# Optimization experiments

Hardware: AMD Instinct MI355X
Metric: run time of the kernel (lower is better)

The kernel has to match this reference:

```python
import jax, jax.numpy as jnp
import numpy as np

# RReLU in eval mode is leaky_relu with slope = (lower+upper)/2 = (1/8 + 1/3)/2
RRELU_SLOPE = (1.0 / 8.0 + 1.0 / 3.0) / 2.0  # = 11/48

N_NODES, FEAT_DIM = 100000, 512
EMBED_DIM = 256
BATCH, NUM_SAMPLE = 16384, 10


def setup_inputs() -> dict:
    key = jax.random.key(0)
    k1, k2, k3 = jax.random.split(key, 3)
    features = jax.random.normal(k1, (N_NODES, FEAT_DIM), dtype=jnp.float32)
    # Xavier-uniform-style init for the weight [embed_dim, feat_dim]
    bound = float(np.sqrt(6.0 / (EMBED_DIM + FEAT_DIM)))
    weight = jax.random.uniform(k2, (EMBED_DIM, FEAT_DIM), dtype=jnp.float32,
                                minval=-bound, maxval=bound)
    # Pre-sampled neighbor ids per batch node: [BATCH, NUM_SAMPLE]
    neigh_idx = jax.random.randint(k3, (BATCH, NUM_SAMPLE), 0, N_NODES, dtype=jnp.int64)
    return {"features": features, "weight": weight, "neigh_idx": neigh_idx}


def reference(features, weight, neigh_idx):
    # Mean aggregator: gather sampled neighbor features and average -> [B, F]
    agg = jnp.take(features, neigh_idx, axis=0).mean(axis=1)
    # weight.mm(agg.t()) -> [E, B]
    y = jnp.einsum("ef,bf->eb", weight, agg)
    # RReLU (eval mode): leaky with mean slope
    return jnp.where(y >= 0, y, y * RRELU_SLOPE)
```

## Files before the change

kernel.cpp:

```cpp
#include <hip/hip_runtime.h>
#include <stdint.h>

constexpr int FEAT  = 512;
constexpr int EMB   = 256;
constexpr int BATCH = 16384;
constexpr int NSAMP = 10;
constexpr int NB    = 32;
constexpr float SLOPE  = 11.0f / 48.0f;
constexpr float INV_NS = 1.0f / 10.0f;

using f32x4 = __attribute__((ext_vector_type(4))) float;
using frag8 = __attribute__((ext_vector_type(8))) short;

static __device__ __forceinline__ unsigned f2b(float x) {
    unsigned u = __builtin_bit_cast(unsigned, x);
    return (u + 0x7fffu + ((u >> 16) & 1u)) >> 16;
}
static __device__ __forceinline__ unsigned pk2(float lo, float hi) {
    return f2b(lo) | (f2b(hi) << 16);
}

__global__ __launch_bounds__(256, 2) void enc_fused(const float* __restrict__ feat,
                                                    const float* __restrict__ wgt,
                                                    const int*   __restrict__ idx,
                                                    float*       __restrict__ out) {
    __shared__ ushort Bs[NB * FEAT];

    const int tid = threadIdx.x;
    const int n0  = blockIdx.x * NB;

    {
        const int r   = tid >> 3;
        const int sub = tid & 7;
        const int* ib = idx + (size_t)(n0 + r) * NSAMP;
        const float* base[NSAMP];
#pragma unroll
        for (int j = 0; j < NSAMP; ++j)
            base[j] = feat + (size_t)ib[j] * FEAT;
        const int swz = (r & 7) << 4;
#pragma unroll
        for (int c = 0; c < 16; ++c) {
            const int col4 = c * 8 + sub;
            float sx = 0.f, sy = 0.f, sz = 0.f, sw = 0.f;
#pragma unroll
            for (int j = 0; j < NSAMP; ++j) {
                const float4 v = *reinterpret_cast<const float4*>(base[j] + col4 * 4);
                sx += v.x; sy += v.y; sz += v.z; sw += v.w;
            }
            ushort4 o;
            o.x = (ushort)f2b(sx * INV_NS); o.y = (ushort)f2b(sy * INV_NS);
            o.z = (ushort)f2b(sz * INV_NS); o.w = (ushort)f2b(sw * INV_NS);
            const int kb = (col4 * 8) ^ swz;
            *reinterpret_cast<ushort4*>((char*)Bs + r * (FEAT * 2) + kb) = o;
        }
    }
    __syncthreads();

    const int wv   = tid >> 6;
    const int lane = tid & 63;
    const int l15  = lane & 15, lq = lane >> 4;
    const int mb   = wv * 64;

    f32x4 acc[4][2] = {};

#pragma unroll
    for (int k0 = 0; k0 < FEAT; k0 += 32) {
        frag8 af[4], bf[2];
#pragma unroll
        for (int i = 0; i < 4; ++i) {
            const float* wp = wgt + (size_t)(mb + i * 16 + l15) * FEAT + k0 + lq * 8;
            const float4 a0 = *reinterpret_cast<const float4*>(wp);
            const float4 a1 = *reinterpret_cast<const float4*>(wp + 4);
            union { frag8 f; unsigned u[4]; } pk;
            pk.u[0] = pk2(a0.x, a0.y);
            pk.u[1] = pk2(a0.z, a0.w);
            pk.u[2] = pk2(a1.x, a1.y);
            pk.u[3] = pk2(a1.z, a1.w);
            af[i] = pk.f;
        }
#pragma unroll
        for (int j = 0; j < 2; ++j) {
            const int row = j * 16 + l15;
            const int kb  = (k0 * 2 + lq * 16) ^ ((row & 7) << 4);
            bf[j] = *reinterpret_cast<const frag8*>((const char*)Bs + row * (FEAT * 2) + kb);
        }
#pragma unroll
        for (int i = 0; i < 4; ++i)
#pragma unroll
            for (int j = 0; j < 2; ++j)
                acc[i][j] = __builtin_amdgcn_mfma_f32_16x16x32_bf16(af[i], bf[j], acc[i][j], 0, 0, 0);
    }

#pragma unroll
    for (int i = 0; i < 4; ++i) {
        const int rb = mb + i * 16 + lq * 4;
#pragma unroll
        for (int j = 0; j < 2; ++j) {
            const int col = n0 + j * 16 + l15;
#pragma unroll
            for (int q = 0; q < 4; ++q) {
                float y = acc[i][j][q];
                y = (y >= 0.f) ? y : y * SLOPE;
                out[(size_t)(rb + q) * BATCH + col] = y;
            }
        }
    }
}

extern "C" void kernel_launch(void* const* d_in, const int* in_sizes, int n_in,
                              void* d_out, int out_size, void* d_ws, size_t ws_size,
                              hipStream_t stream) {
    const float* feat = (const float*)d_in[0];
    const float* wgt  = (const float*)d_in[1];
    const int*   idx  = (const int*)d_in[2];
    float*       out  = (float*)d_out;

    enc_fused<<<BATCH / NB, 256, 0, stream>>>(feat, wgt, idx, out);
}
```

Measured before the change: 75.90 us.

## Double batch tile to 64 nodes with 512 threads and wave-per-row gather

Each block now handles 64 batch nodes with 8 waves instead of 32 nodes with 4 waves. The gather changes so that one wave reads a whole neighbor row as contiguous 32-byte chunks per lane and writes packed bf16 straight to shared memory. The MFMA tiling becomes 32x64 per wave instead of 64x32, so the weight matrix is re-read and re-converted half as often across the grid. The cost is double the LDS per block (64KB), which may limit how many blocks fit on each CU, and half as many blocks in the grid.

```diff
diff --git a/kernel.cpp b/kernel.cpp
--- a/kernel.cpp
+++ b/kernel.cpp
@@ -5,7 +5,7 @@
 constexpr int EMB   = 256;
 constexpr int BATCH = 16384;
 constexpr int NSAMP = 10;
-constexpr int NB    = 32;
+constexpr int NB    = 64;
 constexpr float SLOPE  = 11.0f / 48.0f;
 constexpr float INV_NS = 1.0f / 10.0f;
 
@@ -20,82 +20,78 @@
     return f2b(lo) | (f2b(hi) << 16);
 }
 
-__global__ __launch_bounds__(256, 2) void enc_fused(const float* __restrict__ feat,
+__global__ __launch_bounds__(512, 2) void enc_fused(const float* __restrict__ feat,
                                                     const float* __restrict__ wgt,
                                                     const int*   __restrict__ idx,
                                                     float*       __restrict__ out) {
     __shared__ ushort Bs[NB * FEAT];
 
-    const int tid = threadIdx.x;
-    const int n0  = blockIdx.x * NB;
+    const int tid  = threadIdx.x;
+    const int wv   = tid >> 6;
+    const int lane = tid & 63;
+    const int n0   = blockIdx.x * NB;
 
-    {
-        const int r   = tid >> 3;
-        const int sub = tid & 7;
-        const int* ib = idx + (size_t)(n0 + r) * NSAMP;
-        const float* base[NSAMP];
+#pragma unroll 2
+    for (int rr = 0; rr < 8; ++rr) {
+        const int r  = wv * 8 + rr;
+        const int ru = __builtin_amdgcn_readfirstlane(r);
+        const int* ib = idx + (size_t)(n0 + ru) * NSAMP;
+        f32x4 s0 = {0.f, 0.f, 0.f, 0.f}, s1 = {0.f, 0.f, 0.f, 0.f};
 #pragma unroll
-        for (int j = 0; j < NSAMP; ++j)
-            base[j] = feat + (size_t)ib[j] * FEAT;
-        const int swz = (r & 7) << 4;
-#pragma unroll
-        for (int c = 0; c < 16; ++c) {
-            const int col4 = c * 8 + sub;
-            float sx = 0.f, sy = 0.f, sz = 0.f, sw = 0.f;
-#pragma unroll
-            for (int j = 0; j < NSAMP; ++j) {
-                const float4 v = *reinterpret_cast<const float4*>(base[j] + col4 * 4);
-                sx += v.x; sy += v.y; sz += v.z; sw += v.w;
-            }
-            ushort4 o;
-            o.x = (ushort)f2b(sx * INV_NS); o.y = (ushort)f2b(sy * INV_NS);
-            o.z = (ushort)f2b(sz * INV_NS); o.w = (ushort)f2b(sw * INV_NS);
-            const int kb = (col4 * 8) ^ swz;
-            *reinterpret_cast<ushort4*>((char*)Bs + r * (FEAT * 2) + kb) = o;
+        for (int j = 0; j < NSAMP; ++j) {
+            const float* fp = feat + (size_t)ib[j] * FEAT + lane * 8;
+            const f32x4 v0 = *reinterpret_cast<const f32x4*>(fp);
+            const f32x4 v1 = *reinterpret_cast<const f32x4*>(fp + 4);
+            s0 += v0; s1 += v1;
         }
+        union { frag8 f; unsigned u[4]; } o;
+        o.u[0] = pk2(s0[0] * INV_NS, s0[1] * INV_NS);
+        o.u[1] = pk2(s0[2] * INV_NS, s0[3] * INV_NS);
+        o.u[2] = pk2(s1[0] * INV_NS, s1[1] * INV_NS);
+        o.u[3] = pk2(s1[2] * INV_NS, s1[3] * INV_NS);
+        const int kb = (lane * 16) ^ ((r & 7) << 4);
+        *reinterpret_cast<frag8*>((char*)Bs + r * (FEAT * 2) + kb) = o.f;
     }
     __syncthreads();
 
-    const int wv   = tid >> 6;
-    const int lane = tid & 63;
-    const int l15  = lane & 15, lq = lane >> 4;
-    const int mb   = wv * 64;
+    const int l15 = lane & 15, lq = lane >> 4;
+    const int m0w = wv * 32;
 
-    f32x4 acc[4][2] = {};
+    f32x4 acc[2][4] = {};
 
 #pragma unroll
     for (int k0 = 0; k0 < FEAT; k0 += 32) {
-        frag8 af[4], bf[2];
+        frag8 af[2], bf[4];
 #pragma unroll
-        for (int i = 0; i < 4; ++i) {
-            const float* wp = wgt + (size_t)(mb + i * 16 + l15) * FEAT + k0 + lq * 8;
-            const float4 a0 = *reinterpret_cast<const float4*>(wp);
-            const float4 a1 = *reinterpret_cast<const float4*>(wp + 4);
+        for (int i = 0; i < 2; ++i) {
+            const float* wp = wgt + (size_t)(m0w + i * 16 + l15) * FEAT + k0 + lq * 8;
+            const f32x4 a0 = *reinterpret_cast<const f32x4*>(wp);
+            const f32x4 a1 = *reinterpret_cast<const f32x4*>(wp + 4);
             union { frag8 f; unsigned u[4]; } pk;
-            pk.u[0] = pk2(a0.x, a0.y);
-            pk.u[1] = pk2(a0.z, a0.w);
-            pk.u[2] = pk2(a1.x, a1.y);
-            pk.u[3] = pk2(a1.z, a1.w);
+            pk.u[0] = pk2(a0[0], a0[1]);
+            pk.u[1] = pk2(a0[2], a0[3]);
+            pk.u[2] = pk2(a1[0], a1[1]);
+            pk.u[3] = pk2(a1[2], a1[3]);
             af[i] = pk.f;
         }
 #pragma unroll
-        for (int j = 0; j < 2; ++j) {
+        for (int j = 0; j < 4; ++j) {
             const int row = j * 16 + l15;
             const int kb  = (k0 * 2 + lq * 16) ^ ((row & 7) << 4);
             bf[j] = *reinterpret_cast<const frag8*>((const char*)Bs + row * (FEAT * 2) + kb);
         }
 #pragma unroll
-        for (int i = 0; i < 4; ++i)
+        for (int i = 0; i < 2; ++i)
 #pragma unroll
-            for (int j = 0; j < 2; ++j)
+            for (int j = 0; j < 4; ++j)
                 acc[i][j] = __builtin_amdgcn_mfma_f32_16x16x32_bf16(af[i], bf[j], acc[i][j], 0, 0, 0);
     }
 
 #pragma unroll
-    for (int i = 0; i < 4; ++i) {
-        const int rb = mb + i * 16 + lq * 4;
+    for (int i = 0; i < 2; ++i) {
+        const int rb = m0w + i * 16 + lq * 4;
 #pragma unroll
-        for (int j = 0; j < 2; ++j) {
+        for (int j = 0; j < 4; ++j) {
             const int col = n0 + j * 16 + l15;
 #pragma unroll
             for (int q = 0; q < 4; ++q) {
@@ -115,5 +111,5 @@
     const int*   idx  = (const int*)d_in[2];
     float*       out  = (float*)d_out;
 
-    enc_fused<<<BATCH / NB, 256, 0, stream>>>(feat, wgt, idx, out);
+    enc_fused<<<BATCH / NB, 512, 0, stream>>>(feat, wgt, idx, out);
 }
```

Result: faster. 68.19 us (-10.2%).

## Stream neighbor gathers through per-wave LDS ring via async global_load_lds

Applied to the files above, without the earlier changes.

Replaces the register-based gather of ten neighbor rows with a per-wave 4-deep ring buffer in LDS, filled by async global_load_lds and paced by explicit vmcnt waits. Each wave handles its own 8 batch rows with whole-row contiguous loads, so fetches stay in flight while earlier rows are accumulated. Indices are staged in LDS first, and bf16 packing now uses the HIP intrinsic instead of the manual rounding code. The added 32KB of staging LDS may reduce occupancy, and the hand-written vmcnt counts are fragile.

```diff
diff --git a/kernel.cpp b/kernel.cpp
--- a/kernel.cpp
+++ b/kernel.cpp
@@ -1,4 +1,5 @@
 #include <hip/hip_runtime.h>
+#include <hip/hip_bf16.h>
 #include <stdint.h>
 
 constexpr int FEAT  = 512;
@@ -6,60 +7,86 @@
 constexpr int BATCH = 16384;
 constexpr int NSAMP = 10;
 constexpr int NB    = 32;
+constexpr int NW    = 4;
+constexpr int RPW   = NB / NW;
+constexpr int CH    = RPW * NSAMP;
+constexpr int RING  = 4;
 constexpr float SLOPE  = 11.0f / 48.0f;
 constexpr float INV_NS = 1.0f / 10.0f;
 
 using f32x4 = __attribute__((ext_vector_type(4))) float;
 using frag8 = __attribute__((ext_vector_type(8))) short;
 
-static __device__ __forceinline__ unsigned f2b(float x) {
-    unsigned u = __builtin_bit_cast(unsigned, x);
-    return (u + 0x7fffu + ((u >> 16) & 1u)) >> 16;
-}
-static __device__ __forceinline__ unsigned pk2(float lo, float hi) {
-    return f2b(lo) | (f2b(hi) << 16);
+static __device__ __forceinline__ unsigned bpack2(float a, float b) {
+    __hip_bfloat162 h = __float22bfloat162_rn(make_float2(a, b));
+    unsigned u; __builtin_memcpy(&u, &h, 4);
+    return u;
 }
 
 __global__ __launch_bounds__(256, 2) void enc_fused(const float* __restrict__ feat,
                                                     const float* __restrict__ wgt,
                                                     const int*   __restrict__ idx,
                                                     float*       __restrict__ out) {
+    __shared__ float  Stage[NW][RING][FEAT];
     __shared__ ushort Bs[NB * FEAT];
+    __shared__ int    IdxS[NW][CH];
 
-    const int tid = threadIdx.x;
-    const int n0  = blockIdx.x * NB;
+    const int tid  = threadIdx.x;
+    const int wv   = tid >> 6;
+    const int lane = tid & 63;
+    const int n0   = blockIdx.x * NB;
 
-    {
-        const int r   = tid >> 3;
-        const int sub = tid & 7;
-        const int* ib = idx + (size_t)(n0 + r) * NSAMP;
-        const float* base[NSAMP];
+    for (int f = lane; f < CH; f += 64)
+        IdxS[wv][f] = idx[(size_t)(n0 + wv * RPW) * NSAMP + f];
+
+    auto issue = [&](int f) {
+        const int nbr = IdxS[wv][f];
+        const float* src = feat + (size_t)nbr * FEAT + lane * 4;
+        float* dst = &Stage[wv][f & (RING - 1)][0];
+        __builtin_amdgcn_global_load_lds(
+            (const __attribute__((address_space(1))) void*)src,
+            (__attribute__((address_space(3))) void*)dst, 16, 0, 0);
+        __builtin_amdgcn_global_load_lds(
+            (const __attribute__((address_space(1))) void*)(src + 256),
+            (__attribute__((address_space(3))) void*)(dst + 256), 16, 0, 0);
+    };
+
 #pragma unroll
-        for (int j = 0; j < NSAMP; ++j)
-            base[j] = feat + (size_t)ib[j] * FEAT;
-        const int swz = (r & 7) << 4;
+    for (int f = 0; f < RING; ++f) issue(f);
+
+    f32x4 s0 = {0.f, 0.f, 0.f, 0.f}, s1 = {0.f, 0.f, 0.f, 0.f};
 #pragma unroll
-        for (int c = 0; c < 16; ++c) {
-            const int col4 = c * 8 + sub;
-            float sx = 0.f, sy = 0.f, sz = 0.f, sw = 0.f;
+    for (int rr = 0; rr < RPW; ++rr) {
 #pragma unroll
-            for (int j = 0; j < NSAMP; ++j) {
-                const float4 v = *reinterpret_cast<const float4*>(base[j] + col4 * 4);
-                sx += v.x; sy += v.y; sz += v.z; sw += v.w;
+        for (int j = 0; j < NSAMP; ++j) {
+            const int f = rr * NSAMP + j;
+            if (f <= CH - RING) asm volatile("s_waitcnt vmcnt(6)" ::: "memory");
+            else                asm volatile("s_waitcnt vmcnt(0)" ::: "memory");
+            __builtin_amdgcn_sched_barrier(0);
+            const float* sp = &Stage[wv][f & (RING - 1)][lane * 4];
+            s0 += *reinterpret_cast<const f32x4*>(sp);
+            s1 += *reinterpret_cast<const f32x4*>(sp + 256);
+            __builtin_amdgcn_sched_barrier(0);
+            if (f + RING < CH) issue(f + RING);
+            if (j == NSAMP - 1) {
+                s0 *= INV_NS; s1 *= INV_NS;
+                const int r   = wv * RPW + rr;
+                const int swz = (r & 7) << 4;
+                uint2 lo, hi;
+                lo.x = bpack2(s0[0], s0[1]); lo.y = bpack2(s0[2], s0[3]);
+                hi.x = bpack2(s1[0], s1[1]); hi.y = bpack2(s1[2], s1[3]);
+                char* rowp = (char*)Bs + r * (FEAT * 2);
+                *reinterpret_cast<uint2*>(rowp + ((lane * 8) ^ swz))       = lo;
+                *reinterpret_cast<uint2*>(rowp + ((512 + lane * 8) ^ swz)) = hi;
+                s0 = (f32x4){0.f, 0.f, 0.f, 0.f};
+                s1 = (f32x4){0.f, 0.f, 0.f, 0.f};
             }
-            ushort4 o;
-            o.x = (ushort)f2b(sx * INV_NS); o.y = (ushort)f2b(sy * INV_NS);
-            o.z = (ushort)f2b(sz * INV_NS); o.w = (ushort)f2b(sw * INV_NS);
-            const int kb = (col4 * 8) ^ swz;
-            *reinterpret_cast<ushort4*>((char*)Bs + r * (FEAT * 2) + kb) = o;
         }
     }
     __syncthreads();
 
-    const int wv   = tid >> 6;
-    const int lane = tid & 63;
-    const int l15  = lane & 15, lq = lane >> 4;
-    const int mb   = wv * 64;
+    const int l15 = lane & 15, lq = lane >> 4;
+    const int m0w = wv * 64;
 
     f32x4 acc[4][2] = {};
 
@@ -68,38 +95,36 @@
         frag8 af[4], bf[2];
 #pragma unroll
         for (int i = 0; i < 4; ++i) {
-            const float* wp = wgt + (size_t)(mb + i * 16 + l15) * FEAT + k0 + lq * 8;
-            const float4 a0 = *reinterpret_cast<const float4*>(wp);
-            const float4 a1 = *reinterpret_cast<const float4*>(wp + 4);
-            union { frag8 f; unsigned u[4]; } pk;
-            pk.u[0] = pk2(a0.x, a0.y);
-            pk.u[1] = pk2(a0.z, a0.w);
-            pk.u[2] = pk2(a1.x, a1.y);
-            pk.u[3] = pk2(a1.z, a1.w);
+            const float* wp = wgt + (size_t)(m0w + i * 16 + l15) * FEAT + k0 + lq * 8;
+            const f32x4 a0 = *reinterpret_cast<const f32x4*>(wp);
+            const f32x4 a1 = *reinterpret_cast<const f32x4*>(wp + 4);
+            union { unsigned u[4]; frag8 f; } pk;
+            pk.u[0] = bpack2(a0[0], a0[1]); pk.u[1] = bpack2(a0[2], a0[3]);
+            pk.u[2] = bpack2(a1[0], a1[1]); pk.u[3] = bpack2(a1[2], a1[3]);
             af[i] = pk.f;
         }
 #pragma unroll
-        for (int j = 0; j < 2; ++j) {
-            const int row = j * 16 + l15;
+        for (int jj = 0; jj < 2; ++jj) {
+            const int row = jj * 16 + l15;
             const int kb  = (k0 * 2 + lq * 16) ^ ((row & 7) << 4);
-            bf[j] = *reinterpret_cast<const frag8*>((const char*)Bs + row * (FEAT * 2) + kb);
+            bf[jj] = *reinterpret_cast<const frag8*>((const char*)Bs + row * (FEAT * 2) + kb);
         }
 #pragma unroll
         for (int i = 0; i < 4; ++i)
 #pragma unroll
-            for (int j = 0; j < 2; ++j)
-                acc[i][j] = __builtin_amdgcn_mfma_f32_16x16x32_bf16(af[i], bf[j], acc[i][j], 0, 0, 0);
+            for (int jj = 0; jj < 2; ++jj)
+                acc[i][jj] = __builtin_amdgcn_mfma_f32_16x16x32_bf16(af[i], bf[jj], acc[i][jj], 0, 0, 0);
     }
 
 #pragma unroll
     for (int i = 0; i < 4; ++i) {
-        const int rb = mb + i * 16 + lq * 4;
+        const int rb = m0w + i * 16 + lq * 4;
 #pragma unroll
-        for (int j = 0; j < 2; ++j) {
-            const int col = n0 + j * 16 + l15;
+        for (int jj = 0; jj < 2; ++jj) {
+            const int col = n0 + jj * 16 + l15;
 #pragma unroll
             for (int q = 0; q < 4; ++q) {
-                float y = acc[i][j][q];
+                float y = acc[i][jj][q];
                 y = (y >= 0.f) ? y : y * SLOPE;
                 out[(size_t)(rb + q) * BATCH + col] = y;
             }
```

Result: slower. 82.13 us (+8.2%).
